# Kernel tuning notes

Hardware: AMD Instinct MI355X
Metric: run time of the kernel (lower is better)

Reference implementation:

```python
import jax, jax.numpy as jnp
import numpy as np
from jax import lax

B, T, L, D, K, VOCAB = 64, 128, 32, 128, 64, 50000


def setup_inputs() -> dict:
    key = jax.random.key(0)
    ks = jax.random.split(key, 8)
    prgrph = jax.random.randint(ks[0], (B, T, L), 0, VOCAB, dtype=jnp.int32)
    prgrph_mask = jax.random.randint(ks[1], (B, T, L), 0, 2, dtype=jnp.int32).astype(bool)
    embedding_matrix = jax.random.normal(ks[2], (VOCAB, D), dtype=jnp.float32)
    positional_mask = jax.random.normal(ks[3], (L, D), dtype=jnp.float32)
    Uw = jax.random.normal(ks[4], (D, D), dtype=jnp.float32) * 0.05
    Vw = jax.random.normal(ks[5], (D, D), dtype=jnp.float32) * 0.05
    Ww = jax.random.normal(ks[6], (D, D), dtype=jnp.float32) * 0.05
    keys = jax.random.normal(ks[7], (B, K, D), dtype=jnp.float32)
    return {"prgrph": prgrph, "prgrph_mask": prgrph_mask,
            "embedding_matrix": embedding_matrix, "positional_mask": positional_mask,
            "Uw": Uw, "Vw": Vw, "Ww": Ww, "keys": keys}


def _entity_scan(enc, sent_mask, keys, Uw, Vw, Ww):
    # enc: [B,T,D] encoded sentences; sent_mask: [B,T] bool; keys: [B,K,D]
    h0 = jnp.zeros_like(keys)  # initial entity hidden state = zeros

    def step(h, xs):
        s, m = xs  # s: [B,D], m: [B]
        # Eq 2: gate = sigmoid(s . h + s . k)  -> [B,K]
        g = jax.nn.sigmoid(jnp.einsum('bkd,bd->bk', h + keys, s))
        # Eq 3: h_tilda = sigmoid(h U + k V + s W)  -> [B,K,D]
        h_tilda = jax.nn.sigmoid(
            jnp.einsum('bkd,de->bke', h, Uw)
            + jnp.einsum('bkd,de->bke', keys, Vw)
            + (s @ Ww)[:, None, :])
        # Eq 4-5: add gated update, L2-normalize over embedding dim
        hn = h + g[..., None] * h_tilda
        hn = hn / jnp.sqrt(jnp.maximum(jnp.sum(hn * hn, axis=-1, keepdims=True), 1e-12))
        # only paragraphs with an active sentence at this step are updated
        h = jnp.where(m[:, None, None], hn, h)
        return h, None

    h_last, _ = lax.scan(step, h0, (jnp.swapaxes(enc, 0, 1), sent_mask.T))
    return h_last


def reference(prgrph, prgrph_mask, embedding_matrix, positional_mask, Uw, Vw, Ww, keys):
    # embed words; padded words contribute zero to the sentence encoding
    emb = embedding_matrix[prgrph] * prgrph_mask[..., None].astype(embedding_matrix.dtype)  # [B,T,L,D]
    # Sent_encoder: weighted bag of words with learned positional mask
    enc = jnp.einsum('btld,ld->btd', emb, positional_mask)  # [B,T,D]
    sent_mask = jnp.any(prgrph_mask, axis=2)  # [B,T]
    return _entity_scan(enc, sent_mask, keys, Uw, Vw, Ww)  # [B,K,D]
```

## Files before the change

### kernel.cpp

```cpp
#include <hip/hip_runtime.h>
#include <hip/hip_bf16.h>
#include <stdint.h>

#define B_ 64
#define T_ 128
#define L_ 32
#define D_ 128
#define K_ 64

#define FLAG_OFF  0
#define SM_OFF    256
#define ENCSW_OFF (SM_OFF + B_*T_)
#define KS2_OFF   (ENCSW_OFF + B_*T_*256)
#define KV_OFF    (KS2_OFF + B_*4*T_*16)

typedef __attribute__((ext_vector_type(8))) short short8b;
typedef __attribute__((ext_vector_type(4))) float f32x4;

union frag_cast { uint4 u; short8b s; };

__device__ __forceinline__ float sigmoidf_(float x){ return 1.0f/(1.0f + __expf(-x)); }

__device__ __forceinline__ unsigned short bfb(float x){
  __hip_bfloat16 h = __float2bfloat16(x);
  return __builtin_bit_cast(unsigned short, h);
}
__device__ __forceinline__ float bf2f(unsigned short u){
  return __uint_as_float(((unsigned)u) << 16);
}

__device__ __forceinline__ void gl16(const float* g, float* l){
  __builtin_amdgcn_global_load_lds((const __attribute__((address_space(1))) void*)g,
                                   (__attribute__((address_space(3))) void*)l, 16, 0, 0);
}
__device__ __forceinline__ void gl4(const float* g, float* l){
  __builtin_amdgcn_global_load_lds((const __attribute__((address_space(1))) void*)g,
                                   (__attribute__((address_space(3))) void*)l, 4, 0, 0);
}

__global__ __launch_bounds__(256) void k_detect(const uint8_t* __restrict__ m,
                                                int* __restrict__ flags){
  const unsigned* w = (const unsigned*)m;
  const int base = blockIdx.x * 512;
  unsigned acc = 0;
  acc |= w[base + threadIdx.x]       & 0xFFFFFF00u;
  acc |= w[base + threadIdx.x + 256] & 0xFFFFFF00u;
  int any = __syncthreads_or((int)(acc != 0u));
  if(threadIdx.x == 0) flags[blockIdx.x] = any;
}

__global__ __launch_bounds__(128) void k_enc(const int* __restrict__ prg,
                                             const uint8_t* __restrict__ pm8,
                                             const float* __restrict__ emb,
                                             const float* __restrict__ pos,
                                             const float* __restrict__ Ww,
                                             const float* __restrict__ keys,
                                             float* __restrict__ W){
  const int bt = blockIdx.x;
  const int b  = bt / T_;
  const int t  = bt % T_;
  const int d  = threadIdx.x;
  int myf  = ((const int*)W)[FLAG_OFF + (d & 127)];
  int flag = __syncthreads_or(myf);
  __shared__ float keysl[K_*129];
  __shared__ float encl[D_];
  for(int r=0;r<K_;r++) keysl[r*129 + d] = keys[(b*K_ + r)*D_ + d];
  const int* pmi = (const int*)pm8;
  float acc = 0.f; int anym = 0;
  for(int l=0;l<L_;l++){
    int off = bt*L_ + l;
    int m = flag ? (int)pm8[off] : pmi[off];
    if(m){
      anym = 1;
      int idx = prg[off];
      acc += emb[idx*D_ + d] * pos[l*D_ + d];
    }
  }
  encl[d] = acc;
  W[ENCSW_OFF + bt*256 + d] = acc;
  __syncthreads();
  float sw = 0.f;
  for(int e=0;e<D_;e++) sw += encl[e] * Ww[e*D_ + d];
  W[ENCSW_OFF + bt*256 + 128 + d] = sw;
  if(d < K_){
    float ks = 0.f;
    for(int dd=0;dd<D_;dd++) ks += keysl[d*129 + dd] * encl[dd];
    W[KS2_OFF + ((b*4 + (d>>4))*T_ + t)*16 + (d&15)] = ks;
  }
  if(d==0) W[SM_OFF + bt] = anym ? 1.f : 0.f;
}

__global__ __launch_bounds__(128) void k_kv(const float* __restrict__ keys,
                                            const float* __restrict__ Vw,
                                            float* __restrict__ W){
  const int bk = blockIdx.x;
  const int d  = threadIdx.x;
  __shared__ float kr[D_];
  kr[d] = keys[bk*D_ + d];
  __syncthreads();
  float acc = 0.f;
  for(int e=0;e<D_;e++) acc += kr[e] * Vw[e*D_ + d];
  W[KV_OFF + bk*D_ + d] = acc;
}

__global__ __attribute__((amdgpu_flat_work_group_size(64,64), amdgpu_waves_per_eu(1)))
void k_scan(const float* __restrict__ W,
            const float* __restrict__ Uw,
            float* __restrict__ out){
  const int b    = blockIdx.x >> 2;
  const int kg   = blockIdx.x & 3;
  const int lane = threadIdx.x;
  const int e    = lane & 15;
  const int q    = lane >> 4;

  __shared__ float ring[8*256];
  __shared__ float ksl[T_*16];
  __shared__ float sml[T_];

  short8b ufrag[8][4];
  #pragma unroll
  for(int rt=0; rt<8; ++rt){
    #pragma unroll
    for(int kc=0; kc<4; ++kc){
      const float* r0 = &Uw[(32*kc + 4*q)*D_ + 16*rt + e];
      short8b f;
      #pragma unroll
      for(int j=0;j<8;++j) f[j] = (short)bfb(r0[((j>>2)*16 + (j&3))*D_]);
      ufrag[rt][kc] = f;
    }
  }
  f32x4 kvv[8];
  {
    const float* kvp = &W[KV_OFF + (b*K_ + kg*16 + e)*D_ + 4*q];
    #pragma unroll
    for(int rt=0;rt<8;++rt) kvv[rt] = *(const f32x4*)&kvp[16*rt];
  }
  f32x4 vY[8];
  #pragma unroll
  for(int rt=0;rt<8;++rt) vY[rt] = 0.f;

  const float* ENCSW = &W[ENCSW_OFF + b*T_*256];
  const float* KS2   = &W[KS2_OFF + (b*4 + kg)*T_*16];
  const float* SMg   = &W[SM_OFF + b*T_];

  #pragma unroll
  for(int i=0;i<8;++i) gl16(&KS2[i*256 + lane*4], &ksl[i*256]);
  gl4(&SMg[lane],      &sml[0]);
  gl4(&SMg[64 + lane], &sml[64]);
  #pragma unroll
  for(int s=0;s<7;++s) gl16(&ENCSW[s*256 + lane*4], &ring[s*256]);

  auto dostep = [&](int t){
    int slot = t & 7;
    f32x4 sv[8], sw[8];
    #pragma unroll
    for(int rt=0;rt<8;++rt){
      sv[rt] = *(const f32x4*)&ring[slot*256 +       16*rt + 4*q];
      sw[rt] = *(const f32x4*)&ring[slot*256 + 128 + 16*rt + 4*q];
    }
    float ks = ksl[t*16 + e];
    float sm = sml[t];

    short8b bhi[4], blo[4];
    #pragma unroll
    for(int kc=0;kc<4;++kc){
      const f32x4& va = vY[2*kc];
      const f32x4& vb = vY[2*kc+1];
      unsigned short a0=bfb(va[0]), a1=bfb(va[1]), a2=bfb(va[2]), a3=bfb(va[3]);
      unsigned short b0=bfb(vb[0]), b1=bfb(vb[1]), b2=bfb(vb[2]), b3=bfb(vb[3]);
      frag_cast fh;
      fh.u = make_uint4(((unsigned)a1<<16)|a0, ((unsigned)a3<<16)|a2,
                        ((unsigned)b1<<16)|b0, ((unsigned)b3<<16)|b2);
      unsigned short c0=bfb(va[0]-bf2f(a0)), c1=bfb(va[1]-bf2f(a1));
      unsigned short c2=bfb(va[2]-bf2f(a2)), c3=bfb(va[3]-bf2f(a3));
      unsigned short d0=bfb(vb[0]-bf2f(b0)), d1=bfb(vb[1]-bf2f(b1));
      unsigned short d2=bfb(vb[2]-bf2f(b2)), d3=bfb(vb[3]-bf2f(b3));
      frag_cast fl;
      fl.u = make_uint4(((unsigned)c1<<16)|c0, ((unsigned)c3<<16)|c2,
                        ((unsigned)d1<<16)|d0, ((unsigned)d3<<16)|d2);
      bhi[kc] = fh.s;
      blo[kc] = fl.s;
    }

    float n0=0.f,n1=0.f,n2=0.f,n3=0.f, g0=0.f,g1=0.f,g2=0.f,g3=0.f;
    #pragma unroll
    for(int rt=0;rt<8;++rt){
      n0 += vY[rt][0]*vY[rt][0];  g0 += vY[rt][0]*sv[rt][0];
      n1 += vY[rt][1]*vY[rt][1];  g1 += vY[rt][1]*sv[rt][1];
      n2 += vY[rt][2]*vY[rt][2];  g2 += vY[rt][2]*sv[rt][2];
      n3 += vY[rt][3]*vY[rt][3];  g3 += vY[rt][3]*sv[rt][3];
    }
    float ns = (n0+n1)+(n2+n3);
    float gs = (g0+g1)+(g2+g3);
    ns += __shfl_xor(ns,16);
    ns += __shfl_xor(ns,32);
    gs += __shfl_xor(gs,16);
    gs += __shfl_xor(gs,32);
    float n = rsqrtf(fmaxf(ns, 1e-12f));
    float g = sigmoidf_(fmaf(n, gs, ks));

    f32x4 ah[8], al[8];
    #pragma unroll
    for(int rt=0;rt<8;++rt){ ah[rt] = 0.f; al[rt] = 0.f; }
    #pragma unroll
    for(int rt=0;rt<8;++rt){
      #pragma unroll
      for(int kc=0;kc<4;++kc){
        ah[rt] = __builtin_amdgcn_mfma_f32_16x16x32_bf16(ufrag[rt][kc], bhi[kc], ah[rt], 0,0,0);
        al[rt] = __builtin_amdgcn_mfma_f32_16x16x32_bf16(ufrag[rt][kc], blo[kc], al[rt], 0,0,0);
      }
    }

    bool upd = (sm != 0.f);
    #pragma unroll
    for(int rt=0;rt<8;++rt){
      #pragma unroll
      for(int r=0;r<4;++r){
        float t0 = sw[rt][r] + kvv[rt][r];
        float x  = fmaf(n, ah[rt][r], fmaf(n, al[rt][r], t0));
        float ht = sigmoidf_(x);
        float vn = fmaf(g, ht, n*vY[rt][r]);
        vY[rt][r] = upd ? vn : vY[rt][r];
      }
    }
  };

  #pragma unroll 1
  for(int t=0; t<T_; ++t){
    int r = t+7 < T_ ? t+7 : T_-1;
    gl16(&ENCSW[r*256 + lane*4], &ring[((t+7)&7)*256]);
    asm volatile("s_waitcnt vmcnt(7)" ::: "memory");
    __builtin_amdgcn_sched_barrier(0);
    dostep(t);
  }

  float ns = 0.f;
  #pragma unroll
  for(int rt=0;rt<8;++rt){
    #pragma unroll
    for(int r=0;r<4;++r) ns += vY[rt][r]*vY[rt][r];
  }
  ns += __shfl_xor(ns,16);
  ns += __shfl_xor(ns,32);
  float n = rsqrtf(fmaxf(ns, 1e-12f));
  float* op = &out[(b*K_ + kg*16 + e)*D_ + 4*q];
  #pragma unroll
  for(int rt=0;rt<8;++rt){
    f32x4 o;
    #pragma unroll
    for(int r=0;r<4;++r) o[r] = vY[rt][r]*n;
    *(f32x4*)&op[16*rt] = o;
  }
}

extern "C" void kernel_launch(void* const* d_in, const int* in_sizes, int n_in,
                              void* d_out, int out_size, void* d_ws, size_t ws_size,
                              hipStream_t stream) {
  const int*     prg  = (const int*)d_in[0];
  const uint8_t* pm   = (const uint8_t*)d_in[1];
  const float*   emb  = (const float*)d_in[2];
  const float*   pos  = (const float*)d_in[3];
  const float*   Uw   = (const float*)d_in[4];
  const float*   Vw   = (const float*)d_in[5];
  const float*   Ww   = (const float*)d_in[6];
  const float*   keys = (const float*)d_in[7];
  float* W   = (float*)d_ws;
  float* out = (float*)d_out;

  hipLaunchKernelGGL(k_detect, dim3(128),    dim3(256), 0, stream, pm, (int*)d_ws + FLAG_OFF);
  hipLaunchKernelGGL(k_enc,    dim3(B_*T_),  dim3(128), 0, stream, prg, pm, emb, pos, Ww, keys, W);
  hipLaunchKernelGGL(k_kv,     dim3(B_*K_),  dim3(128), 0, stream, keys, Vw, W);
  hipLaunchKernelGGL(k_scan,   dim3(B_*4),   dim3(64),  0, stream, W, Uw, out);
}
```

Before: 528.0 us.

## Spread scan over more blocks with two entities per block

The scan kernel now launches 32 blocks per batch instead of 4, and each wavefront handles only 2 entities. The 16 MFMA columns hold those 2 entities replicated 8 times, so most of the matrix work is redundant. The per-entity key·sentence values get a new [B,K,T] layout that needs only one small LDS preload, and waves_per_eu is raised to 2. The aim is to cut the long serial per-step latency by filling more CUs (2048 blocks instead of 256), at the cost of far more redundant MFMA work and repeated loads of Uw. Sigmoid and rsqrt also switch to the hardware rcp/rsq builtins.

New measurement: 844.3 us. 59.9% more time.

```diff
diff --git a/kernel.cpp b/kernel.cpp
--- a/kernel.cpp
+++ b/kernel.cpp
@@ -11,15 +11,17 @@
 #define FLAG_OFF  0
 #define SM_OFF    256
 #define ENCSW_OFF (SM_OFF + B_*T_)
-#define KS2_OFF   (ENCSW_OFF + B_*T_*256)
-#define KV_OFF    (KS2_OFF + B_*4*T_*16)
+#define KS3_OFF   (ENCSW_OFF + B_*T_*256)
+#define KV_OFF    (KS3_OFF + B_*K_*T_)
 
 typedef __attribute__((ext_vector_type(8))) short short8b;
 typedef __attribute__((ext_vector_type(4))) float f32x4;
 
 union frag_cast { uint4 u; short8b s; };
 
-__device__ __forceinline__ float sigmoidf_(float x){ return 1.0f/(1.0f + __expf(-x)); }
+__device__ __forceinline__ float frcp_(float x){ return __builtin_amdgcn_rcpf(x); }
+__device__ __forceinline__ float frsq_(float x){ return __builtin_amdgcn_rsqf(x); }
+__device__ __forceinline__ float sigmoidf_(float x){ return frcp_(1.0f + __expf(-x)); }
 
 __device__ __forceinline__ unsigned short bfb(float x){
   __hip_bfloat16 h = __float2bfloat16(x);
@@ -85,7 +87,7 @@
   if(d < K_){
     float ks = 0.f;
     for(int dd=0;dd<D_;dd++) ks += keysl[d*129 + dd] * encl[dd];
-    W[KS2_OFF + ((b*4 + (d>>4))*T_ + t)*16 + (d&15)] = ks;
+    W[KS3_OFF + (b*K_ + d)*T_ + t] = ks;
   }
   if(d==0) W[SM_OFF + bt] = anym ? 1.f : 0.f;
 }
@@ -103,18 +105,19 @@
   W[KV_OFF + bk*D_ + d] = acc;
 }
 
-__global__ __attribute__((amdgpu_flat_work_group_size(64,64), amdgpu_waves_per_eu(1)))
+__global__ __attribute__((amdgpu_flat_work_group_size(64,64), amdgpu_waves_per_eu(2)))
 void k_scan(const float* __restrict__ W,
             const float* __restrict__ Uw,
             float* __restrict__ out){
-  const int b    = blockIdx.x >> 2;
-  const int kg   = blockIdx.x & 3;
+  const int b    = blockIdx.x >> 5;
+  const int p    = blockIdx.x & 31;
   const int lane = threadIdx.x;
   const int e    = lane & 15;
   const int q    = lane >> 4;
+  const int ent  = 2*p + (e & 1);
 
   __shared__ float ring[8*256];
-  __shared__ float ksl[T_*16];
+  __shared__ float ksl2[256];
   __shared__ float sml[T_];
 
   short8b ufrag[8][4];
@@ -131,7 +134,7 @@
   }
   f32x4 kvv[8];
   {
-    const float* kvp = &W[KV_OFF + (b*K_ + kg*16 + e)*D_ + 4*q];
+    const float* kvp = &W[KV_OFF + (b*K_ + ent)*D_ + 4*q];
     #pragma unroll
     for(int rt=0;rt<8;++rt) kvv[rt] = *(const f32x4*)&kvp[16*rt];
   }
@@ -140,11 +143,10 @@
   for(int rt=0;rt<8;++rt) vY[rt] = 0.f;
 
   const float* ENCSW = &W[ENCSW_OFF + b*T_*256];
-  const float* KS2   = &W[KS2_OFF + (b*4 + kg)*T_*16];
+  const float* KS3   = &W[KS3_OFF + (b*K_ + 2*p)*T_];
   const float* SMg   = &W[SM_OFF + b*T_];
 
-  #pragma unroll
-  for(int i=0;i<8;++i) gl16(&KS2[i*256 + lane*4], &ksl[i*256]);
+  gl16(&KS3[lane*4], ksl2);
   gl4(&SMg[lane],      &sml[0]);
   gl4(&SMg[64 + lane], &sml[64]);
   #pragma unroll
@@ -158,7 +160,7 @@
       sv[rt] = *(const f32x4*)&ring[slot*256 +       16*rt + 4*q];
       sw[rt] = *(const f32x4*)&ring[slot*256 + 128 + 16*rt + 4*q];
     }
-    float ks = ksl[t*16 + e];
+    float ks = ksl2[(e&1)*128 + t];
     float sm = sml[t];
 
     short8b bhi[4], blo[4];
@@ -196,7 +198,7 @@
     ns += __shfl_xor(ns,32);
     gs += __shfl_xor(gs,16);
     gs += __shfl_xor(gs,32);
-    float n = rsqrtf(fmaxf(ns, 1e-12f));
+    float n = frsq_(fmaxf(ns, 1e-12f));
     float g = sigmoidf_(fmaf(n, gs, ks));
 
     f32x4 ah[8], al[8];
@@ -242,14 +244,16 @@
   }
   ns += __shfl_xor(ns,16);
   ns += __shfl_xor(ns,32);
-  float n = rsqrtf(fmaxf(ns, 1e-12f));
-  float* op = &out[(b*K_ + kg*16 + e)*D_ + 4*q];
-  #pragma unroll
-  for(int rt=0;rt<8;++rt){
-    f32x4 o;
-    #pragma unroll
-    for(int r=0;r<4;++r) o[r] = vY[rt][r]*n;
-    *(f32x4*)&op[16*rt] = o;
+  float n = frsq_(fmaxf(ns, 1e-12f));
+  if(e < 2){
+    float* op = &out[(b*K_ + 2*p + e)*D_ + 4*q];
+    #pragma unroll
+    for(int rt=0;rt<8;++rt){
+      f32x4 o;
+      #pragma unroll
+      for(int r=0;r<4;++r) o[r] = vY[rt][r]*n;
+      *(f32x4*)&op[16*rt] = o;
+    }
   }
 }
 
@@ -270,5 +274,5 @@
   hipLaunchKernelGGL(k_detect, dim3(128),    dim3(256), 0, stream, pm, (int*)d_ws + FLAG_OFF);
   hipLaunchKernelGGL(k_enc,    dim3(B_*T_),  dim3(128), 0, stream, prg, pm, emb, pos, Ww, keys, W);
   hipLaunchKernelGGL(k_kv,     dim3(B_*K_),  dim3(128), 0, stream, keys, Vw, W);
-  hipLaunchKernelGGL(k_scan,   dim3(B_*4),   dim3(64),  0, stream, W, Uw, out);
-}
+  hipLaunchKernelGGL(k_scan,   dim3(B_*32),  dim3(64),  0, stream, W, Uw, out);
+}
```
